# Performance work log

Hardware: AMD Instinct MI355X
Metric: run time of the kernel (lower is better)

The kernel has to match this reference:

```python
import jax, jax.numpy as jnp
import numpy as np

D_MODEL = 768
D_HEAD = 64
N_HEADS = D_MODEL // D_HEAD


def setup_inputs() -> dict:
    key = jax.random.key(0)
    k1, k2, k3 = jax.random.split(key, 3)
    n, h, w = 2, 48, 48
    x = jax.random.normal(k1, (n, h, w, D_MODEL), dtype=jnp.float32)
    # torch Linear weights: [out_features, in_features]
    w_qkv = jax.random.normal(k2, (3 * D_MODEL, D_MODEL), dtype=jnp.float32) * (D_MODEL ** -0.5)
    w_out = jax.random.normal(k3, (D_MODEL, D_MODEL), dtype=jnp.float32) * (D_MODEL ** -0.5)
    return {"x": x, "w_qkv": w_qkv, "w_out": w_out, "kernel_size": 7}


def _natten_mask(h: int, w: int, kernel_size: int) -> jnp.ndarray:
    # Faithful to _natten_mask_mod: q_x = idx // w, q_y = idx % w,
    # both axes compared against the same kernel_size.
    idx = jnp.arange(h * w)
    qx, qy = idx // w, idx % w
    horiz = jnp.abs(qx[:, None] - qx[None, :]) <= kernel_size
    vert = jnp.abs(qy[:, None] - qy[None, :]) <= kernel_size
    return horiz & vert  # [hw, hw] bool


def reference(x, w_qkv, w_out, kernel_size):
    n, h, w, d = x.shape
    hw = h * w
    qkv = jnp.einsum('nhwd,fd->nhwf', x, w_qkv)  # [n, h, w, 3*d]
    qkv = qkv.reshape(n, hw, 3, N_HEADS, D_HEAD)
    q = jnp.transpose(qkv[:, :, 0], (0, 2, 1, 3))  # [n, nh, hw, e]
    k = jnp.transpose(qkv[:, :, 1], (0, 2, 1, 3))
    v = jnp.transpose(qkv[:, :, 2], (0, 2, 1, 3))

    mask = _natten_mask(h, w, kernel_size)  # [hw, hw]
    scale = D_HEAD ** -0.5
    scores = jnp.einsum('bnqe,bnke->bnqk', q, k) * scale
    neg = jnp.asarray(jnp.finfo(scores.dtype).min, scores.dtype)
    scores = jnp.where(mask[None, None], scores, neg)
    attn = jax.nn.softmax(scores, axis=-1)
    o = jnp.einsum('bnqk,bnke->bnqe', attn, v)  # [n, nh, hw, e]
    o = jnp.transpose(o, (0, 2, 1, 3)).reshape(n, h, w, d)
    return jnp.einsum('nhwd,fd->nhwf', o, w_out)
```

## Files before the change

### kernel.cpp

```cpp
#include <hip/hip_runtime.h>

using f32x4 = __attribute__((ext_vector_type(4))) float;
using h8v   = __attribute__((ext_vector_type(8))) _Float16;
using h4v   = __attribute__((ext_vector_type(4))) _Float16;
using s8v   = __attribute__((ext_vector_type(8))) short;

#define MFMAH(a, b, c)   __builtin_amdgcn_mfma_f32_16x16x32_f16((a), (b), (c), 0, 0, 0)
#define MFMAH16(a, b, c) __builtin_amdgcn_mfma_f32_16x16x16f16((a), (b), (c), 0, 0, 0)

typedef __attribute__((address_space(3))) unsigned int lds_uint;
typedef const __attribute__((address_space(1))) unsigned int glb_uint;
__device__ inline void gload16(void* l, const void* g) {
    __builtin_amdgcn_global_load_lds((glb_uint*)g, (lds_uint*)l, 16, 0, 0);
}

__device__ inline float exp2_fast(float x) {
    float r;
    asm("v_exp_f32 %0, %1" : "=v"(r) : "v"(x));
    return r;
}

__global__ __launch_bounds__(256) void conv_all(const float* __restrict__ x,
                                                const float* __restrict__ wq,
                                                const float* __restrict__ wo,
                                                _Float16* __restrict__ xh,
                                                _Float16* __restrict__ wqh,
                                                _Float16* __restrict__ woh) {
    const int i = blockIdx.x * blockDim.x + threadIdx.x;
    const float* src;
    _Float16* dst;
    int off;
    if (i < 442368)      { src = x;  dst = xh;  off = i; }
    else if (i < 663552) { src = wq; dst = wqh; off = i - 442368; }
    else                 { src = wo; dst = woh; off = i - 663552; }
    const float4 a = *(const float4*)(src + (size_t)off * 8);
    const float4 b = *(const float4*)(src + (size_t)off * 8 + 4);
    h8v h;
    h[0] = (_Float16)a.x; h[1] = (_Float16)a.y; h[2] = (_Float16)a.z; h[3] = (_Float16)a.w;
    h[4] = (_Float16)b.x; h[5] = (_Float16)b.y; h[6] = (_Float16)b.z; h[7] = (_Float16)b.w;
    *(h8v*)(dst + (size_t)off * 8) = h;
}

__global__ __launch_bounds__(256) void gemm_qkv_f16(const _Float16* __restrict__ A,
                                                    const _Float16* __restrict__ B,
                                                    _Float16* __restrict__ C,
                                                    _Float16* __restrict__ vt) {
    constexpr int LD = 768, LDC = 2304;
    __shared__ __align__(16) _Float16 sA[128][64], sB[128][64];
    const int b = blockIdx.x;
    const int sb = (b & 7) * 81 + (b >> 3);
    const int bx = sb % 18, by = sb / 18;
    const int m0 = by * 128, n0 = bx * 128;
    const int tid = threadIdx.x, lane = tid & 63, wv = tid >> 6;
    const int wm = (wv >> 1) * 64, wn = (wv & 1) * 64;
    const int fr = lane & 15, fkb = (lane >> 4) * 8;

    const int srow = tid >> 3, scol = (tid & 7) * 8;
    const _Float16* gA = A + (size_t)(m0 + srow) * LD + scol;
    const _Float16* gB = B + (size_t)(n0 + srow) * LD + scol;

    f32x4 acc[4][4];
#pragma unroll
    for (int m = 0; m < 4; ++m)
#pragma unroll
        for (int n2 = 0; n2 < 4; ++n2) acc[m][n2] = (f32x4){0.f, 0.f, 0.f, 0.f};

    for (int kt = 0; kt < 12; ++kt) {
        const int k0 = kt * 64;
#pragma unroll
        for (int q = 0; q < 4; ++q) {
            gload16(&sA[q * 32 + srow][scol], gA + (size_t)(q * 32) * LD + k0);
            gload16(&sB[q * 32 + srow][scol], gB + (size_t)(q * 32) * LD + k0);
        }
        __syncthreads();

#pragma unroll
        for (int kk = 0; kk < 2; ++kk) {
            h8v fa[4], fb[4];
#pragma unroll
            for (int m = 0; m < 4; ++m) fa[m] = *(const h8v*)&sA[wm + m * 16 + fr][kk * 32 + fkb];
#pragma unroll
            for (int n2 = 0; n2 < 4; ++n2) fb[n2] = *(const h8v*)&sB[wn + n2 * 16 + fr][kk * 32 + fkb];
#pragma unroll
            for (int m = 0; m < 4; ++m)
#pragma unroll
                for (int n2 = 0; n2 < 4; ++n2) acc[m][n2] = MFMAH(fa[m], fb[n2], acc[m][n2]);
        }
        __syncthreads();
    }

    const int rg = (lane >> 4) * 4;
    if (bx < 12) {
#pragma unroll
        for (int m = 0; m < 4; ++m)
#pragma unroll
            for (int n2 = 0; n2 < 4; ++n2)
#pragma unroll
                for (int r = 0; r < 4; ++r)
                    C[(size_t)(m0 + wm + m * 16 + rg + r) * LDC + (n0 + wn + n2 * 16 + fr)] =
                        (_Float16)acc[m][n2][r];
    } else {
        const int nb = m0 / 2304;
        const int tokb = m0 - nb * 2304 + wm + rg;
#pragma unroll
        for (int m = 0; m < 4; ++m)
#pragma unroll
            for (int n2 = 0; n2 < 4; ++n2) {
                const int f = n0 - 1536 + wn + n2 * 16 + fr;
                const int head = f >> 6, e = f & 63;
                h4v v;
#pragma unroll
                for (int r = 0; r < 4; ++r) v[r] = (_Float16)acc[m][n2][r];
                *(h4v*)(vt + (size_t)((nb * 12 + head) * 64 + e) * 2304 + tokb + m * 16) = v;
            }
    }
}

__global__ __launch_bounds__(192) void attn_flash(const _Float16* __restrict__ qkv,
                                                  const _Float16* __restrict__ vt,
                                                  _Float16* __restrict__ o,
                                                  const int* __restrict__ ksp) {
    __shared__ __align__(16) char sbuf[2][28672];
    const int tid = threadIdx.x;
    const int lane = tid & 63, wv = tid >> 6;
    const int fr = lane & 15, fg = lane >> 4;

    const int b = blockIdx.x;
    const int xcd = b & 7, g = b >> 3;
    const int qx = xcd * 6 + g / 24;
    const int hn = g % 24;
    const int head = hn >> 1, n = hn & 1;
    const int KS = *ksp;

    const int krow0 = tid >> 3, kc = tid & 7;
    const int vrow0 = tid / 6,  vc = tid % 6;
    const int ksw = (krow0 & 7) << 4;
    const int vsw = (vrow0 & 7) << 4;

    const int qy = wv * 16 + fr;
    const _Float16* qrow = qkv + (size_t)(n * 2304 + qx * 48 + qy) * 2304 + head * 64;
    h8v qa0 = *(const h8v*)(qrow + fg * 8);
    h8v qa1 = *(const h8v*)(qrow + 32 + fg * 8);
    qa0 = qa0 * (_Float16)0.1803368801f;
    qa1 = qa1 * (_Float16)0.1803368801f;

    int nt0 = (wv * 16 - KS) >> 4;      if (nt0 < 0) nt0 = 0;
    int nt1 = (wv * 16 + 15 + KS) >> 4; if (nt1 > 2) nt1 = 2;

    f32x4 mbias[3];
#pragma unroll
    for (int nt = 0; nt < 3; ++nt)
#pragma unroll
        for (int r = 0; r < 4; ++r) {
            const int dy = nt * 16 + fg * 4 + r - qy;
            mbias[nt][r] = (dy < -KS || dy > KS) ? -1e4f : 0.f;
        }

    f32x4 Oacc[4];
#pragma unroll
    for (int e = 0; e < 4; ++e) Oacc[e] = (f32x4){0.f, 0.f, 0.f, 0.f};
    float rs_acc = 0.f;

    const int lo = (qx - KS) > 0 ? (qx - KS) : 0;
    const int hi = (qx + KS) < 47 ? (qx + KS) : 47;

    const _Float16* kgbase = qkv + (size_t)(n * 2304) * 2304 + 768 + head * 64;
    const _Float16* vgbase = vt + (size_t)((n * 12 + head) * 64) * 2304;

    auto loadrow = [&](int kx, s8v& k0, s8v& k1, s8v& v0, s8v& v1) {
        const _Float16* kg = kgbase + (size_t)(kx * 48) * 2304;
        const _Float16* vg = vgbase + kx * 48;
        k0 = *(const s8v*)(kg + (size_t)krow0 * 2304 + kc * 8);
        k1 = *(const s8v*)(kg + (size_t)(krow0 + 24) * 2304 + kc * 8);
        v0 = *(const s8v*)(vg + (size_t)vrow0 * 2304 + vc * 8);
        v1 = *(const s8v*)(vg + (size_t)(vrow0 + 32) * 2304 + vc * 8);
    };
    auto storerow = [&](char* d, s8v k0, s8v k1, s8v v0, s8v v1) {
        *(s8v*)(d + krow0 * 128 + ((kc * 16) ^ ksw)) = k0;
        *(s8v*)(d + (krow0 + 24) * 128 + ((kc * 16) ^ ksw)) = k1;
        *(s8v*)(d + 6144 + vrow0 * 128 + ((vc * 16) ^ vsw)) = v0;
        *(s8v*)(d + 6144 + (vrow0 + 32) * 128 + ((vc * 16) ^ vsw)) = v1;
    };
    auto computeRow = [&](const char* base) {
        const char* K = base;
        const char* V = base + 6144;
        f32x4 s[3];
#pragma unroll
        for (int nt = 0; nt < 3; ++nt)
            if (nt >= nt0 && nt <= nt1) {
                const int rr = nt * 16 + fr;
                const int sw = (rr & 7) << 4;
                const h8v kb0 = *(const h8v*)(K + rr * 128 + ((fg * 16) ^ sw));
                const h8v kb1 = *(const h8v*)(K + rr * 128 + ((64 + fg * 16) ^ sw));
                f32x4 z = MFMAH(kb0, qa0, mbias[nt]);
                z = MFMAH(kb1, qa1, z);
                s[nt] = z;
            }
#pragma unroll
        for (int nt = 0; nt < 3; ++nt)
            if (nt >= nt0 && nt <= nt1) {
                h4v pa;
#pragma unroll
                for (int r = 0; r < 4; ++r) {
                    const float pv = exp2_fast(s[nt][r]);
                    rs_acc += pv;
                    pa[r] = (_Float16)pv;
                }
                const int slot = nt * 2 + (fg >> 1), off8 = (fg & 1) * 8;
#pragma unroll
                for (int et = 0; et < 4; ++et) {
                    const int rv = et * 16 + fr;
                    const h4v vb = *(const h4v*)(V + rv * 128 +
                                                 (((slot ^ (rv & 7)) << 4) + off8));
                    Oacc[et] = MFMAH16(vb, pa, Oacc[et]);
                }
            }
    };

    {
        s8v k0, k1, v0, v1;
        loadrow(lo, k0, k1, v0, v1);
        storerow(sbuf[0], k0, k1, v0, v1);
        if (lo + 1 <= hi) {
            loadrow(lo + 1, k0, k1, v0, v1);
            storerow(sbuf[0] + 14336, k0, k1, v0, v1);
        }
    }

    int p = 0;
    for (int kx = lo; kx <= hi; kx += 2) {
        __syncthreads();
        const bool pre0 = (kx + 2 <= hi), pre1 = (kx + 3 <= hi);
        s8v a0, a1, b0, b1, c0, c1, d0, d1;
        if (pre0) loadrow(kx + 2, a0, a1, b0, b1);
        if (pre1) loadrow(kx + 3, c0, c1, d0, d1);

        __builtin_amdgcn_s_setprio(1);
        computeRow(sbuf[p]);
        if (kx + 1 <= hi) computeRow(sbuf[p] + 14336);
        __builtin_amdgcn_s_setprio(0);

        if (pre0) storerow(sbuf[p ^ 1], a0, a1, b0, b1);
        if (pre1) storerow(sbuf[p ^ 1] + 14336, c0, c1, d0, d1);
        p ^= 1;
    }

    rs_acc += __shfl_xor(rs_acc, 16);
    rs_acc += __shfl_xor(rs_acc, 32);
    const float linv = 1.f / rs_acc;
    _Float16* ob = o + (size_t)(n * 2304 + qx * 48 + wv * 16 + fr) * 768 + head * 64;
#pragma unroll
    for (int et = 0; et < 4; ++et) {
        h4v ov;
#pragma unroll
        for (int r = 0; r < 4; ++r) ov[r] = (_Float16)(Oacc[et][r] * linv);
        *(h4v*)(ob + et * 16 + fg * 4) = ov;
    }
}

__global__ __launch_bounds__(256) void gemm_out_f16(const _Float16* __restrict__ A,
                                                    const _Float16* __restrict__ B,
                                                    float* __restrict__ C) {
    constexpr int LD = 768, LDC = 768;
    __shared__ __align__(16) _Float16 sA[128][64], sB[128][64];
    const int b = blockIdx.x;
    const int sb = (b & 7) * 27 + (b >> 3);
    const int bx = sb % 6, by = sb / 6;
    const int m0 = by * 128, n0 = bx * 128;
    const int tid = threadIdx.x, lane = tid & 63, wv = tid >> 6;
    const int wm = (wv >> 1) * 64, wn = (wv & 1) * 64;
    const int fr = lane & 15, fkb = (lane >> 4) * 8;

    const int srow = tid >> 3, scol = (tid & 7) * 8;
    const _Float16* gA = A + (size_t)(m0 + srow) * LD + scol;
    const _Float16* gB = B + (size_t)(n0 + srow) * LD + scol;

    f32x4 acc[4][4];
#pragma unroll
    for (int m = 0; m < 4; ++m)
#pragma unroll
        for (int n2 = 0; n2 < 4; ++n2) acc[m][n2] = (f32x4){0.f, 0.f, 0.f, 0.f};

    for (int kt = 0; kt < 12; ++kt) {
        const int k0 = kt * 64;
#pragma unroll
        for (int q = 0; q < 4; ++q) {
            gload16(&sA[q * 32 + srow][scol], gA + (size_t)(q * 32) * LD + k0);
            gload16(&sB[q * 32 + srow][scol], gB + (size_t)(q * 32) * LD + k0);
        }
        __syncthreads();

#pragma unroll
        for (int kk = 0; kk < 2; ++kk) {
            h8v fa[4], fb[4];
#pragma unroll
            for (int m = 0; m < 4; ++m) fa[m] = *(const h8v*)&sA[wm + m * 16 + fr][kk * 32 + fkb];
#pragma unroll
            for (int n2 = 0; n2 < 4; ++n2) fb[n2] = *(const h8v*)&sB[wn + n2 * 16 + fr][kk * 32 + fkb];
#pragma unroll
            for (int m = 0; m < 4; ++m)
#pragma unroll
                for (int n2 = 0; n2 < 4; ++n2) acc[m][n2] = MFMAH(fa[m], fb[n2], acc[m][n2]);
        }
        __syncthreads();
    }

    const int rg = (lane >> 4) * 4;
#pragma unroll
    for (int m = 0; m < 4; ++m)
#pragma unroll
        for (int n2 = 0; n2 < 4; ++n2)
#pragma unroll
            for (int r = 0; r < 4; ++r)
                C[(size_t)(m0 + wm + m * 16 + rg + r) * LDC + (n0 + wn + n2 * 16 + fr)] =
                    acc[m][n2][r];
}

extern "C" void kernel_launch(void* const* d_in, const int* in_sizes, int n_in,
                              void* d_out, int out_size, void* d_ws, size_t ws_size,
                              hipStream_t stream) {
    const float* x     = (const float*)d_in[0];
    const float* w_qkv = (const float*)d_in[1];
    const float* w_out = (const float*)d_in[2];
    const int*   ksp   = (const int*)d_in[3];
    float* out = (float*)d_out;

    char* ws = (char*)d_ws;
    _Float16* qkv = (_Float16*)(ws);
    _Float16* vt  = (_Float16*)(ws + 21237760);
    _Float16* o   = (_Float16*)(ws + 28315648);
    _Float16* xh  = (_Float16*)(ws + 35393536);
    _Float16* wqh = (_Float16*)(ws + 42471424);
    _Float16* woh = (_Float16*)(ws + 46010368);

    conv_all<<<dim3(2880), 256, 0, stream>>>(x, w_qkv, w_out, xh, wqh, woh);
    gemm_qkv_f16<<<dim3(648), 256, 0, stream>>>(xh, wqh, qkv, vt);
    attn_flash<<<dim3(1152), 192, 0, stream>>>(qkv, vt, o, ksp);
    gemm_out_f16<<<dim3(216), 256, 0, stream>>>(o, woh, out);
}
```

Baseline: 97.72 us.

## Restructure attention K/V pipeline to single-row steps with register prefetch

```diff
diff --git a/kernel.cpp b/kernel.cpp
--- a/kernel.cpp
+++ b/kernel.cpp
@@ -120,7 +120,7 @@
                                                   const _Float16* __restrict__ vt,
                                                   _Float16* __restrict__ o,
                                                   const int* __restrict__ ksp) {
-    __shared__ __align__(16) char sbuf[2][28672];
+    __shared__ __align__(16) char sbuf[2][14336];
     const int tid = threadIdx.x;
     const int lane = tid & 63, wv = tid >> 6;
     const int fr = lane & 15, fg = lane >> 4;
@@ -181,9 +181,27 @@
         *(s8v*)(d + 6144 + vrow0 * 128 + ((vc * 16) ^ vsw)) = v0;
         *(s8v*)(d + 6144 + (vrow0 + 32) * 128 + ((vc * 16) ^ vsw)) = v1;
     };
-    auto computeRow = [&](const char* base) {
-        const char* K = base;
-        const char* V = base + 6144;
+
+    s8v tk0, tk1, tv0, tv1;
+    {
+        s8v a0, a1, b0, b1;
+        loadrow(lo, a0, a1, b0, b1);
+        storerow(sbuf[0], a0, a1, b0, b1);
+        if (lo + 1 <= hi) loadrow(lo + 1, tk0, tk1, tv0, tv1);
+    }
+
+    int p = 0;
+    for (int kx = lo; kx <= hi; ++kx) {
+        __syncthreads();
+        if (kx < hi)
+            storerow(sbuf[p ^ 1], tk0, tk1, tv0, tv1);
+        if (kx + 1 < hi)
+            loadrow(kx + 2, tk0, tk1, tv0, tv1);
+
+        const char* K = sbuf[p];
+        const char* V = sbuf[p] + 6144;
+        __builtin_amdgcn_s_setprio(1);
+
         f32x4 s[3];
 #pragma unroll
         for (int nt = 0; nt < 3; ++nt)
@@ -196,6 +214,7 @@
                 z = MFMAH(kb1, qa1, z);
                 s[nt] = z;
             }
+
 #pragma unroll
         for (int nt = 0; nt < 3; ++nt)
             if (nt >= nt0 && nt <= nt1) {
@@ -215,33 +234,7 @@
                     Oacc[et] = MFMAH16(vb, pa, Oacc[et]);
                 }
             }
-    };
-
-    {
-        s8v k0, k1, v0, v1;
-        loadrow(lo, k0, k1, v0, v1);
-        storerow(sbuf[0], k0, k1, v0, v1);
-        if (lo + 1 <= hi) {
-            loadrow(lo + 1, k0, k1, v0, v1);
-            storerow(sbuf[0] + 14336, k0, k1, v0, v1);
-        }
-    }
-
-    int p = 0;
-    for (int kx = lo; kx <= hi; kx += 2) {
-        __syncthreads();
-        const bool pre0 = (kx + 2 <= hi), pre1 = (kx + 3 <= hi);
-        s8v a0, a1, b0, b1, c0, c1, d0, d1;
-        if (pre0) loadrow(kx + 2, a0, a1, b0, b1);
-        if (pre1) loadrow(kx + 3, c0, c1, d0, d1);
-
-        __builtin_amdgcn_s_setprio(1);
-        computeRow(sbuf[p]);
-        if (kx + 1 <= hi) computeRow(sbuf[p] + 14336);
         __builtin_amdgcn_s_setprio(0);
-
-        if (pre0) storerow(sbuf[p ^ 1], a0, a1, b0, b1);
-        if (pre1) storerow(sbuf[p ^ 1] + 14336, c0, c1, d0, d1);
         p ^= 1;
     }
 
```

Result: faster. 83.20 us (-14.9%).
